# Kernel tuning notes

Measured on AMD Instinct MI355X. Metric: run time of the kernel, lower is better.

Reference implementation:

```python
import jax, jax.numpy as jnp
import numpy as np

IMAGE_H, IMAGE_W = 256, 704
Z, Y, X = 128, 8, 128
BOUNDS = (-50.0, 50.0, -5.0, 5.0, -50.0, 50.0)
CENTROID = (0.0, 1.0, 0.0)
EPS_MEAN = 1e-6
EPS_DEPTH = 1e-4


def _compose_rt(R, t):
    M = jnp.zeros(R.shape[:-2] + (4, 4), R.dtype)
    M = M.at[..., :3, :3].set(R)
    M = M.at[..., :3, 3].set(t)
    M = M.at[..., 3, 3].set(1.0)
    return M


def _safe_inverse(M):
    R = M[..., :3, :3]
    t = M[..., :3, 3]
    Rt = jnp.swapaxes(R, -1, -2)
    return _compose_rt(Rt, -jnp.einsum('...ij,...j->...i', Rt, t))


def _apply_4x4(M, xyz):
    # M: (...,4,4), xyz: (...,N,3) -> (...,N,3)
    return jnp.einsum('...ij,...nj->...ni', M[..., :3, :3], xyz) + M[..., None, :3, 3]


def _xyz_camA():
    # Mem2Ref of gridcloud3d: x_ref = x_mem*vox + MIN + vox/2 (bounds shifted by centroid)
    xmin = BOUNDS[0] + CENTROID[0]; xmax = BOUNDS[1] + CENTROID[0]
    ymin = BOUNDS[2] + CENTROID[1]; ymax = BOUNDS[3] + CENTROID[1]
    zmin = BOUNDS[4] + CENTROID[2]; zmax = BOUNDS[5] + CENTROID[2]
    vx = (xmax - xmin) / X; vy = (ymax - ymin) / Y; vz = (zmax - zmin) / Z
    zz, yy, xx = jnp.meshgrid(jnp.arange(Z, dtype=jnp.float32),
                              jnp.arange(Y, dtype=jnp.float32),
                              jnp.arange(X, dtype=jnp.float32), indexing='ij')
    x = xx * vx + xmin + vx / 2.0
    y = yy * vy + ymin + vy / 2.0
    z = zz * vz + zmin + vz / 2.0
    return jnp.stack([x, y, z], -1).reshape(Z * Y * X, 3)  # mem order (Z,Y,X)


def _bilinear_sample(img, px, py):
    # img: (C,H,W); px,py: (N,) pixel coords; zeros padding (grid_sample align_corners=False)
    C, H, W = img.shape
    x0 = jnp.floor(px); y0 = jnp.floor(py)
    dx = px - x0; dy = py - y0
    x0i = x0.astype(jnp.int32); y0i = y0.astype(jnp.int32)
    flat = img.reshape(C, H * W)

    def gather(yi, xi, w):
        inb = (xi >= 0) & (xi < W) & (yi >= 0) & (yi < H)
        idx = jnp.clip(yi, 0, H - 1) * W + jnp.clip(xi, 0, W - 1)
        return flat[:, idx] * (w * inb.astype(img.dtype))

    return (gather(y0i, x0i, (1 - dx) * (1 - dy))
            + gather(y0i, x0i + 1, dx * (1 - dy))
            + gather(y0i + 1, x0i, (1 - dx) * dy)
            + gather(y0i + 1, x0i + 1, dx * dy))  # (C,N)


def _forward(cam_feat, camera2ego, cam_intrinsic, conv_w):
    B, S, C, Hf, Wf = cam_feat.shape
    # velo_T_cams = merge_rt(camera2ego R, t); cam0_T_camXs = inv(velo_T_cams[:,0]) @ velo_T_cams
    velo_T_cams = _compose_rt(camera2ego[..., :3, :3], camera2ego[..., :3, 3])
    cam0_T_velo = _safe_inverse(velo_T_cams[:, 0])
    cam0_T_camXs = jnp.einsum('bij,bsjk->bsik', cam0_T_velo, velo_T_cams)
    camXs_T_cam0 = _safe_inverse(cam0_T_camXs)
    # scale_intrinsics with sy = Hf/H*0.284, sx = Wf/W*0.44
    sy = Hf / float(IMAGE_H) * 0.284
    sx = Wf / float(IMAGE_W) * 0.44
    fx = cam_intrinsic[..., 0, 0] * sx
    fy = cam_intrinsic[..., 1, 1] * sy
    cx = cam_intrinsic[..., 0, 2] * sx
    cy = cam_intrinsic[..., 1, 2] * sy
    K = jnp.zeros((B, S, 4, 4), cam_feat.dtype)
    K = K.at[..., 0, 0].set(fx).at[..., 1, 1].set(fy)
    K = K.at[..., 0, 2].set(cx).at[..., 1, 2].set(cy)
    K = K.at[..., 2, 2].set(1.0).at[..., 3, 3].set(1.0)
    pixB_T_cam0 = jnp.einsum('bsij,bsjk->bsik', K, camXs_T_cam0)

    xyz = _xyz_camA()  # (N,3), N = Z*Y*X
    xyz_camB = _apply_4x4(camXs_T_cam0, xyz[None, None])  # (B,S,N,3)
    z_cam = xyz_camB[..., 2]
    xyz_pix = _apply_4x4(pixB_T_cam0, xyz[None, None])
    depth = jnp.maximum(xyz_pix[..., 2], EPS_DEPTH)
    x_pix = xyz_pix[..., 0] / depth
    y_pix = xyz_pix[..., 1] / depth
    valid = ((x_pix > -0.5) & (x_pix < Wf - 0.5)
             & (y_pix > -0.5) & (y_pix < Hf - 0.5)
             & (z_cam > 0.0)).astype(cam_feat.dtype)
    # normalize_grid2d (clamp [-2,2]) then grid_sample align_corners=False unnormalize
    gx = jnp.clip(2.0 * x_pix / (Wf - 1) - 1.0, -2.0, 2.0)
    gy = jnp.clip(2.0 * y_pix / (Hf - 1) - 1.0, -2.0, 2.0)
    px = ((gx + 1.0) * Wf - 1.0) / 2.0
    py = ((gy + 1.0) * Hf - 1.0) / 2.0

    feats = cam_feat.reshape(B * S, C, Hf, Wf)
    vals = jax.vmap(_bilinear_sample)(feats, px.reshape(B * S, -1), py.reshape(B * S, -1))
    vals = vals.reshape(B, S, C, -1) * valid[:, :, None, :]  # (B,S,C,N)
    mask = (jnp.abs(vals) > 0).astype(vals.dtype)
    feat_mem = jnp.sum(vals * mask, axis=1) / (EPS_MEAN + jnp.sum(mask, axis=1))  # (B,C,N)
    feat_mem = feat_mem.reshape(B, C, Z, Y, X)

    # BEV compress: permute(0,1,3,2,4) -> (B, C*Y, Z, X), conv3x3 (no bias), InstanceNorm2d, GELU
    feat_bev = jnp.transpose(feat_mem, (0, 1, 3, 2, 4)).reshape(B, C * Y, Z, X)
    out = jax.lax.conv_general_dilated(feat_bev, conv_w, (1, 1), ((1, 1), (1, 1)),
                                       dimension_numbers=('NCHW', 'OIHW', 'NCHW'))
    mu = jnp.mean(out, axis=(2, 3), keepdims=True)
    var = jnp.var(out, axis=(2, 3), keepdims=True)
    out = (out - mu) / jnp.sqrt(var + 1e-5)
    return jax.nn.gelu(out, approximate=False)


def setup_inputs() -> dict:
    key = jax.random.key(0)
    k1, k2, k3 = jax.random.split(key, 3)
    B, S, C, Hf, Wf = 1, 6, 128, 32, 88
    cam_feat = jax.random.normal(k1, (B, S, C, Hf, Wf), jnp.float32)
    # rigid camera2ego: yaw rotations about the y axis + small translations
    yaws = jnp.arange(S, dtype=jnp.float32) * (2.0 * jnp.pi / S)
    c, s = jnp.cos(yaws), jnp.sin(yaws)
    zr, on = jnp.zeros_like(c), jnp.ones_like(c)
    R = jnp.stack([jnp.stack([c, zr, s], -1),
                   jnp.stack([zr, on, zr], -1),
                   jnp.stack([-s, zr, c], -1)], -2)  # (S,3,3)
    t = jax.random.normal(k2, (S, 3), jnp.float32) * 0.5
    cam2ego = jnp.zeros((B, S, 4, 4), jnp.float32)
    cam2ego = cam2ego.at[0, :, :3, :3].set(R).at[0, :, :3, 3].set(t).at[0, :, 3, 3].set(1.0)
    K = jnp.zeros((B, S, 4, 4), jnp.float32)
    K = K.at[..., 0, 0].set(600.0).at[..., 1, 1].set(600.0)
    K = K.at[..., 0, 2].set(352.0).at[..., 1, 2].set(128.0)
    K = K.at[..., 2, 2].set(1.0).at[..., 3, 3].set(1.0)
    conv_w = jax.random.normal(k3, (128, 128 * Y, 3, 3), jnp.float32) / np.sqrt(128 * Y * 9.0).astype(np.float32)
    return {"cam_feat": cam_feat, "camera2ego": cam2ego, "cam_intrinsic": K, "conv_w": conv_w}


def reference(cam_feat, camera2ego, cam_intrinsic, conv_w):
    return _forward(cam_feat, camera2ego, cam_intrinsic, conv_w)
```

## Files before the change

### kernel.cpp

```cpp
#include <hip/hip_runtime.h>
#include <hip/hip_bf16.h>
#include <math.h>

#define HF 32
#define WF 88
#define NCAM 6
#define CC 128
#define ZD 128
#define YD 8
#define XD 128

using f32x4  = __attribute__((ext_vector_type(4))) float;
using bf16x8 = __attribute__((ext_vector_type(8))) short;

#define OFF_P    0ull
#define OFF_W    512ull
#define OFF_CAMT (OFF_W + 2359296ull)
#define OFF_F    (OFF_CAMT + 8650752ull)
#define OFF_CONV (OFF_F + 34611200ull)

__global__ __launch_bounds__(64) void k0_mats(const float* __restrict__ cam2ego,
                                              const float* __restrict__ intr,
                                              float* __restrict__ P) {
  int s = threadIdx.x;
  if (s >= NCAM) return;
  const float* M0 = cam2ego;
  const float* Ms = cam2ego + s * 16;
  float Rb[9], tb[3];
  for (int i = 0; i < 3; i++)
    for (int j = 0; j < 3; j++) {
      float v = 0.f;
      for (int k = 0; k < 3; k++) v += Ms[k * 4 + i] * M0[k * 4 + j];
      Rb[i * 3 + j] = v;
    }
  for (int i = 0; i < 3; i++) {
    float v = 0.f;
    for (int k = 0; k < 3; k++) v += Ms[k * 4 + i] * (M0[k * 4 + 3] - Ms[k * 4 + 3]);
    tb[i] = v;
  }
  const float* Ks = intr + s * 16;
  const float sx = (float)WF / 704.0f * 0.44f;
  const float sy = (float)HF / 256.0f * 0.284f;
  const float fx = Ks[0] * sx, fy = Ks[5] * sy;
  const float cx = Ks[2] * sx, cy = Ks[6] * sy;
  float* p = P + s * 12;
  for (int j = 0; j < 3; j++) p[j]     = fx * Rb[j]     + cx * Rb[6 + j];
  p[3]  = fx * tb[0] + cx * tb[2];
  for (int j = 0; j < 3; j++) p[4 + j] = fy * Rb[3 + j] + cy * Rb[6 + j];
  p[7]  = fy * tb[1] + cy * tb[2];
  for (int j = 0; j < 3; j++) p[8 + j] = Rb[6 + j];
  p[11] = tb[2];
}

__global__ __launch_bounds__(256) void k1_transpose(const float* __restrict__ feat,
                                                    __hip_bfloat16* __restrict__ camT) {
  __shared__ float tile[128 * 89];
  const int b = blockIdx.x;
  const int s = b >> 5;
  const int hrow = b & 31;
  const int t = threadIdx.x;
  for (int idx = t; idx < 128 * 88; idx += 256) {
    const int c = idx / 88;
    const int w = idx - c * 88;
    tile[c * 89 + w] = feat[((size_t)(s * CC + c) * HF + hrow) * WF + w];
  }
  __syncthreads();
  const int c = t & 127;
  const int wh = t >> 7;
  for (int i = 0; i < 44; i++) {
    const int w = i * 2 + wh;
    camT[((size_t)(s * HF + hrow) * WF + w) * CC + c] =
        __float2bfloat16(tile[c * 89 + w]);
  }
}

__global__ __launch_bounds__(256) void k1b_packw(const float* __restrict__ w,
                                                 __hip_bfloat16* __restrict__ wp) {
  const int t = blockIdx.x * 256 + threadIdx.x;
  float v[9];
  #pragma unroll
  for (int d = 0; d < 9; d++) v[d] = w[(size_t)t * 9 + d];
  #pragma unroll
  for (int d = 0; d < 9; d++) wp[(size_t)d * 131072 + t] = __float2bfloat16(v[d]);
}

struct Rec { int off[4]; float w[4]; };

__global__ __launch_bounds__(256) void k2_sample(const __hip_bfloat16* __restrict__ camT,
                                                 const float* __restrict__ P,
                                                 __hip_bfloat16* __restrict__ F) {
  const int bz = blockIdx.x / 65;
  const int bxp = blockIdx.x % 65;
  const int t = threadIdx.x;
  const int sub = t >> 7;
  const int u = t & 127;
  const int bx = bxp * 2 + sub;
  const int zi = bz - 1, xi = bx - 1;
  const int cq = (u & 31) << 2;
  const int yq = u >> 5;
  __hip_bfloat16* Fb = F + ((size_t)bz * 130 + bx) * 1024;
  const bool inplay = !(zi < 0 || zi >= ZD || xi < 0 || xi >= XD);

  __shared__ Rec recs[2][48];
  __shared__ unsigned ymask[2][8];
  const int lane = t & 63;
  const int wv = t >> 6;
  bool vflag = false;
  if ((wv == 0 || wv == 2) && lane < 48 && inplay) {
    const int y = lane / 6, s = lane - y * 6;
    const float* pp = P + s * 12;
    const float vx = 100.0f / 128.0f;
    const float xw = xi * vx - 50.0f + vx * 0.5f;
    const float zw = zi * vx - 50.0f + vx * 0.5f;
    const float yw = y * 1.25f - 4.0f + 0.625f;
    const float zc = pp[8] * xw + pp[9] * yw + pp[10] * zw + pp[11];
    const float xp = pp[0] * xw + pp[1] * yw + pp[2] * zw + pp[3];
    const float yp = pp[4] * xw + pp[5] * yw + pp[6] * zw + pp[7];
    const float dep = fmaxf(zc, 1e-4f);
    const float pxf = xp / dep, pyf = yp / dep;
    const bool valid = (pxf > -0.5f && pxf < (float)WF - 0.5f &&
                        pyf > -0.5f && pyf < (float)HF - 0.5f && zc > 0.0f);
    const float px = pxf * ((float)WF / (float)(WF - 1)) - 0.5f;
    const float py = pyf * ((float)HF / (float)(HF - 1)) - 0.5f;
    const float fx0 = floorf(px), fy0 = floorf(py);
    const float ddx = px - fx0, ddy = py - fy0;
    const int x0i = (int)fx0, y0i = (int)fy0;
    const float vf = valid ? 1.0f : 0.0f;
    float ww[4];
    ww[0] = (1.0f - ddx) * (1.0f - ddy) * vf;
    ww[1] = ddx * (1.0f - ddy) * vf;
    ww[2] = (1.0f - ddx) * ddy * vf;
    ww[3] = ddx * ddy * vf;
    const int cxs[4] = {x0i, x0i + 1, x0i, x0i + 1};
    const int cys[4] = {y0i, y0i, y0i + 1, y0i + 1};
    Rec r;
    float wsum = 0.f;
    #pragma unroll
    for (int k = 0; k < 4; k++) {
      const bool inb = ((unsigned)cxs[k] < WF) && ((unsigned)cys[k] < HF);
      const int xc = min(max(cxs[k], 0), WF - 1);
      const int yc = min(max(cys[k], 0), HF - 1);
      r.w[k] = inb ? ww[k] : 0.0f;
      r.off[k] = (s * (HF * WF) + yc * WF + xc) * CC;
      wsum += r.w[k];
    }
    recs[sub][lane] = r;
    vflag = wsum > 0.0f;
  }
  if (wv == 0 || wv == 2) {
    unsigned long long m = __ballot(vflag);
    if (lane < 8) ymask[wv >> 1][lane] = (unsigned)((m >> (6 * lane)) & 63ull);
  }
  __syncthreads();

  if (!inplay) {
    #pragma unroll
    for (int j = 0; j < 4; j++)
      *reinterpret_cast<unsigned*>(Fb + (cq + j) * 8 + yq * 2) = 0u;
    return;
  }

  float num[2][4] = {{0.f, 0.f, 0.f, 0.f}, {0.f, 0.f, 0.f, 0.f}};
  int cnt[2] = {0, 0};
  #pragma unroll
  for (int yi = 0; yi < 2; yi++) {
    const int y = yq * 2 + yi;
    unsigned ms = ymask[sub][y];
    while (ms) {
      const int s = __builtin_ctz(ms);
      ms &= ms - 1;
      const Rec r = recs[sub][y * 6 + s];
      #pragma unroll
      for (int k = 0; k < 4; k++) {
        const ushort4 uv = *reinterpret_cast<const ushort4*>(&camT[r.off[k] + cq]);
        num[yi][0] += r.w[k] * __bfloat162float(*reinterpret_cast<const __hip_bfloat16*>(&uv.x));
        num[yi][1] += r.w[k] * __bfloat162float(*reinterpret_cast<const __hip_bfloat16*>(&uv.y));
        num[yi][2] += r.w[k] * __bfloat162float(*reinterpret_cast<const __hip_bfloat16*>(&uv.z));
        num[yi][3] += r.w[k] * __bfloat162float(*reinterpret_cast<const __hip_bfloat16*>(&uv.w));
      }
      cnt[yi]++;
    }
  }
  const float inv0 = 1.0f / (1e-6f + (float)cnt[0]);
  const float inv1 = 1.0f / (1e-6f + (float)cnt[1]);
  #pragma unroll
  for (int j = 0; j < 4; j++) {
    __hip_bfloat16 o[2];
    o[0] = __float2bfloat16(num[0][j] * inv0);
    o[1] = __float2bfloat16(num[1][j] * inv1);
    *reinterpret_cast<unsigned*>(Fb + (cq + j) * 8 + yq * 2) =
        *reinterpret_cast<const unsigned*>(o);
  }
}

__device__ __forceinline__ void load_lds16(const void* g, void* l) {
  __builtin_amdgcn_global_load_lds(
      (const __attribute__((address_space(1))) unsigned int*)g,
      (__attribute__((address_space(3))) unsigned int*)l, 16, 0, 0);
}

#define K3_NT 72

__global__ __launch_bounds__(512) void k3_gemm(const __hip_bfloat16* __restrict__ F,
                                               const __hip_bfloat16* __restrict__ Wp,
                                               float* __restrict__ out0,
                                               float* __restrict__ out1) {
  const int orig = (blockIdx.x & 7) * 32 + (blockIdx.x >> 3);
  const int z = orig & 127;
  const int h = orig >> 7;
  const int ciH = h << 9;
  const int tid = threadIdx.x;
  const int w = tid >> 6;
  const int l = tid & 63;
  const int kk = w >> 2;
  const int wq = w & 3;
  const int wm = wq >> 1;
  const int wn = wq & 1;
  __shared__ __hip_bfloat16 lds[4][16384];

  f32x4 acc[4][4];
  #pragma unroll
  for (int m = 0; m < 4; m++)
    #pragma unroll
    for (int n = 0; n < 4; n++)
      acc[m][n] = (f32x4){0.f, 0.f, 0.f, 0.f};

  auto stage = [&](int kt) {
    const int buf = kt & 3;
    const int d = kt >> 3;
    const int dz = d / 3, dx = d - dz * 3;
    const int ci0 = ciH + ((kt & 7) << 6);
    const int zbase = (z + dz) * 130 + dx;
    #pragma unroll
    for (int i = 0; i < 2; i++) {
      const int n = w * 128 + i * 64 + l;
      const int row = n >> 3;
      const int q = (n & 7) ^ (row & 7);
      const __hip_bfloat16* src = F + ((size_t)(zbase + row) << 10) + ci0 + (q << 3);
      load_lds16(src, &lds[buf][(w * 128 + i * 64) * 8]);
    }
    #pragma unroll
    for (int i = 0; i < 2; i++) {
      const int n = w * 128 + i * 64 + l;
      const int co = n >> 3;
      const int q = (n & 7) ^ (co & 7);
      const __hip_bfloat16* src = Wp + ((size_t)d << 17) + ((size_t)co << 10) + ci0 + (q << 3);
      load_lds16(src, &lds[buf][8192 + (w * 128 + i * 64) * 8]);
    }
  };

  auto compute = [&](int kt) {
    const int buf = kt & 3;
    const int r16 = l & 15;
    const int hi = l >> 4;
    const int c = kk * 4 + hi;
    bf16x8 a[4], b[4];
    #pragma unroll
    for (int m = 0; m < 4; m++) {
      const int r = wm * 64 + m * 16 + r16;
      const int slot = c ^ (r & 7);
      a[m] = *reinterpret_cast<const bf16x8*>(&lds[buf][r * 64 + slot * 8]);
    }
    #pragma unroll
    for (int n = 0; n < 4; n++) {
      const int co = wn * 64 + n * 16 + r16;
      const int slot = c ^ (co & 7);
      b[n] = *reinterpret_cast<const bf16x8*>(&lds[buf][8192 + co * 64 + slot * 8]);
    }
    #pragma unroll
    for (int m = 0; m < 4; m++)
      #pragma unroll
      for (int n = 0; n < 4; n++)
        acc[m][n] = __builtin_amdgcn_mfma_f32_16x16x32_bf16(a[m], b[n], acc[m][n], 0, 0, 0);
  };

  stage(0); stage(1); stage(2);

  for (int t = 0; t < K3_NT - 2; ++t) {
    asm volatile("s_waitcnt vmcnt(8)" ::: "memory");
    __builtin_amdgcn_s_barrier();
    if (t + 3 < K3_NT) stage(t + 3);
    compute(t);
  }
  asm volatile("s_waitcnt vmcnt(4)" ::: "memory");
  __builtin_amdgcn_s_barrier();
  compute(K3_NT - 2);
  asm volatile("s_waitcnt vmcnt(0)" ::: "memory");
  __builtin_amdgcn_s_barrier();
  compute(K3_NT - 1);

  float* red = reinterpret_cast<float*>(&lds[0][0]);
  if (kk == 1) {
    float* dst = red + wq * 4096;
    #pragma unroll
    for (int m = 0; m < 4; m++)
      #pragma unroll
      for (int n = 0; n < 4; n++)
        *reinterpret_cast<f32x4*>(&dst[(m * 4 + n) * 256 + l * 4]) = acc[m][n];
  }
  __syncthreads();
  if (kk == 0) {
    const float* srcr = red + wq * 4096;
    float* outP = h ? out1 : out0;
    const int r16 = l & 15;
    const int hi = l >> 4;
    #pragma unroll
    for (int m = 0; m < 4; m++) {
      const int xr = wm * 64 + m * 16 + hi * 4;
      #pragma unroll
      for (int n = 0; n < 4; n++) {
        f32x4 o = *reinterpret_cast<const f32x4*>(&srcr[(m * 4 + n) * 256 + l * 4]);
        f32x4 r = acc[m][n] + o;
        const int co = wn * 64 + n * 16 + r16;
        *reinterpret_cast<f32x4*>(&outP[((size_t)co << 14) + (z << 7) + xr]) = r;
      }
    }
  }
}

__device__ __forceinline__ float gelu_exact(float x) {
  return 0.5f * x * (1.0f + erff(x * 0.70710678118654752440f));
}

__global__ __launch_bounds__(1024) void k4_ln(const float* __restrict__ c0,
                                              const float* __restrict__ c1,
                                              float* __restrict__ outp) {
  const int co = blockIdx.x;
  const int t = threadIdx.x;
  const float4* p0 = reinterpret_cast<const float4*>(c0 + ((size_t)co << 14));
  const float4* p1 = reinterpret_cast<const float4*>(c1 + ((size_t)co << 14));
  float4 v[4];
  float s = 0.f, s2 = 0.f;
  #pragma unroll
  for (int i = 0; i < 4; i++) {
    float4 a = p0[t + (i << 10)];
    float4 b = p1[t + (i << 10)];
    float4 r;
    r.x = a.x + b.x; r.y = a.y + b.y; r.z = a.z + b.z; r.w = a.w + b.w;
    v[i] = r;
    s  += r.x + r.y + r.z + r.w;
    s2 += r.x * r.x + r.y * r.y + r.z * r.z + r.w * r.w;
  }
  #pragma unroll
  for (int off = 32; off > 0; off >>= 1) {
    s  += __shfl_down(s, off);
    s2 += __shfl_down(s2, off);
  }
  __shared__ float red[32];
  __shared__ float mb[2];
  const int wv = t >> 6, ln = t & 63;
  if (ln == 0) { red[wv] = s; red[wv + 16] = s2; }
  __syncthreads();
  if (t == 0) {
    float S = 0.f, S2 = 0.f;
    #pragma unroll
    for (int i = 0; i < 16; i++) { S += red[i]; S2 += red[i + 16]; }
    float mu = S * (1.0f / 16384.0f);
    float var = S2 * (1.0f / 16384.0f) - mu * mu;
    mb[0] = mu;
    mb[1] = 1.0f / sqrtf(var + 1e-5f);
  }
  __syncthreads();
  const float mu = mb[0], inv = mb[1];
  float4* op = reinterpret_cast<float4*>(outp + ((size_t)co << 14));
  #pragma unroll
  for (int i = 0; i < 4; i++) {
    float4 x = v[i];
    float4 r;
    r.x = gelu_exact((x.x - mu) * inv);
    r.y = gelu_exact((x.y - mu) * inv);
    r.z = gelu_exact((x.z - mu) * inv);
    r.w = gelu_exact((x.w - mu) * inv);
    op[t + (i << 10)] = r;
  }
}

extern "C" void kernel_launch(void* const* d_in, const int* in_sizes, int n_in,
                              void* d_out, int out_size, void* d_ws, size_t ws_size,
                              hipStream_t stream) {
  const float* cam_feat = (const float*)d_in[0];
  const float* cam2ego  = (const float*)d_in[1];
  const float* intr     = (const float*)d_in[2];
  const float* conv_w   = (const float*)d_in[3];
  float* out = (float*)d_out;
  char* ws = (char*)d_ws;

  float*          P     = (float*)(ws + OFF_P);
  __hip_bfloat16* Wp    = (__hip_bfloat16*)(ws + OFF_W);
  __hip_bfloat16* camT  = (__hip_bfloat16*)(ws + OFF_CAMT);
  __hip_bfloat16* F     = (__hip_bfloat16*)(ws + OFF_F);
  float*          conv0 = (float*)(ws + OFF_CONV);
  float*          conv1 = (float*)(ws + OFF_CAMT);

  hipLaunchKernelGGL(k0_mats, dim3(1), dim3(64), 0, stream, cam2ego, intr, P);
  hipLaunchKernelGGL(k1_transpose, dim3(NCAM * HF), dim3(256), 0, stream, cam_feat, camT);
  hipLaunchKernelGGL(k1b_packw, dim3(512), dim3(256), 0, stream, conv_w, Wp);
  hipLaunchKernelGGL(k2_sample, dim3(130 * 65), dim3(256), 0, stream, camT, P, F);
  hipLaunchKernelGGL(k3_gemm, dim3(256), dim3(512), 0, stream, F, Wp, conv0, conv1);
  hipLaunchKernelGGL(k4_ln, dim3(128), dim3(1024), 0, stream, conv0, conv1, out);
}
```

Baseline: 111.1 us.

## Merge preprocessing kernels and interleave GEMM staging with split MFMA phases

```diff
diff --git a/kernel.cpp b/kernel.cpp
--- a/kernel.cpp
+++ b/kernel.cpp
@@ -19,69 +19,69 @@
 #define OFF_F    (OFF_CAMT + 8650752ull)
 #define OFF_CONV (OFF_F + 34611200ull)
 
-__global__ __launch_bounds__(64) void k0_mats(const float* __restrict__ cam2ego,
-                                              const float* __restrict__ intr,
-                                              float* __restrict__ P) {
-  int s = threadIdx.x;
-  if (s >= NCAM) return;
-  const float* M0 = cam2ego;
-  const float* Ms = cam2ego + s * 16;
-  float Rb[9], tb[3];
-  for (int i = 0; i < 3; i++)
-    for (int j = 0; j < 3; j++) {
-      float v = 0.f;
-      for (int k = 0; k < 3; k++) v += Ms[k * 4 + i] * M0[k * 4 + j];
-      Rb[i * 3 + j] = v;
-    }
-  for (int i = 0; i < 3; i++) {
-    float v = 0.f;
-    for (int k = 0; k < 3; k++) v += Ms[k * 4 + i] * (M0[k * 4 + 3] - Ms[k * 4 + 3]);
-    tb[i] = v;
-  }
-  const float* Ks = intr + s * 16;
-  const float sx = (float)WF / 704.0f * 0.44f;
-  const float sy = (float)HF / 256.0f * 0.284f;
-  const float fx = Ks[0] * sx, fy = Ks[5] * sy;
-  const float cx = Ks[2] * sx, cy = Ks[6] * sy;
-  float* p = P + s * 12;
-  for (int j = 0; j < 3; j++) p[j]     = fx * Rb[j]     + cx * Rb[6 + j];
-  p[3]  = fx * tb[0] + cx * tb[2];
-  for (int j = 0; j < 3; j++) p[4 + j] = fy * Rb[3 + j] + cy * Rb[6 + j];
-  p[7]  = fy * tb[1] + cy * tb[2];
-  for (int j = 0; j < 3; j++) p[8 + j] = Rb[6 + j];
-  p[11] = tb[2];
-}
-
-__global__ __launch_bounds__(256) void k1_transpose(const float* __restrict__ feat,
-                                                    __hip_bfloat16* __restrict__ camT) {
+__global__ __launch_bounds__(256) void k_pre(const float* __restrict__ feat,
+                                             const float* __restrict__ conv_w,
+                                             const float* __restrict__ cam2ego,
+                                             const float* __restrict__ intr,
+                                             __hip_bfloat16* __restrict__ camT,
+                                             __hip_bfloat16* __restrict__ wp,
+                                             float* __restrict__ P) {
   __shared__ float tile[128 * 89];
   const int b = blockIdx.x;
-  const int s = b >> 5;
-  const int hrow = b & 31;
   const int t = threadIdx.x;
-  for (int idx = t; idx < 128 * 88; idx += 256) {
-    const int c = idx / 88;
-    const int w = idx - c * 88;
-    tile[c * 89 + w] = feat[((size_t)(s * CC + c) * HF + hrow) * WF + w];
-  }
-  __syncthreads();
-  const int c = t & 127;
-  const int wh = t >> 7;
-  for (int i = 0; i < 44; i++) {
-    const int w = i * 2 + wh;
-    camT[((size_t)(s * HF + hrow) * WF + w) * CC + c] =
-        __float2bfloat16(tile[c * 89 + w]);
-  }
-}
-
-__global__ __launch_bounds__(256) void k1b_packw(const float* __restrict__ w,
-                                                 __hip_bfloat16* __restrict__ wp) {
-  const int t = blockIdx.x * 256 + threadIdx.x;
-  float v[9];
-  #pragma unroll
-  for (int d = 0; d < 9; d++) v[d] = w[(size_t)t * 9 + d];
-  #pragma unroll
-  for (int d = 0; d < 9; d++) wp[(size_t)d * 131072 + t] = __float2bfloat16(v[d]);
+  if (b < 192) {
+    const int s = b >> 5;
+    const int hrow = b & 31;
+    for (int idx = t; idx < 128 * 88; idx += 256) {
+      const int c = idx / 88;
+      const int w = idx - c * 88;
+      tile[c * 89 + w] = feat[((size_t)(s * CC + c) * HF + hrow) * WF + w];
+    }
+    __syncthreads();
+    const int c = t & 127;
+    const int wh = t >> 7;
+    for (int i = 0; i < 44; i++) {
+      const int w = i * 2 + wh;
+      camT[((size_t)(s * HF + hrow) * WF + w) * CC + c] =
+          __float2bfloat16(tile[c * 89 + w]);
+    }
+  } else if (b < 704) {
+    const int tt = (b - 192) * 256 + t;
+    float v[9];
+    #pragma unroll
+    for (int d = 0; d < 9; d++) v[d] = conv_w[(size_t)tt * 9 + d];
+    #pragma unroll
+    for (int d = 0; d < 9; d++) wp[(size_t)d * 131072 + tt] = __float2bfloat16(v[d]);
+  } else {
+    const int s = t;
+    if (s >= NCAM) return;
+    const float* M0 = cam2ego;
+    const float* Ms = cam2ego + s * 16;
+    float Rb[9], tb[3];
+    for (int i = 0; i < 3; i++)
+      for (int j = 0; j < 3; j++) {
+        float v = 0.f;
+        for (int k = 0; k < 3; k++) v += Ms[k * 4 + i] * M0[k * 4 + j];
+        Rb[i * 3 + j] = v;
+      }
+    for (int i = 0; i < 3; i++) {
+      float v = 0.f;
+      for (int k = 0; k < 3; k++) v += Ms[k * 4 + i] * (M0[k * 4 + 3] - Ms[k * 4 + 3]);
+      tb[i] = v;
+    }
+    const float* Ks = intr + s * 16;
+    const float sx = (float)WF / 704.0f * 0.44f;
+    const float sy = (float)HF / 256.0f * 0.284f;
+    const float fx = Ks[0] * sx, fy = Ks[5] * sy;
+    const float cx = Ks[2] * sx, cy = Ks[6] * sy;
+    float* p = P + s * 12;
+    for (int j = 0; j < 3; j++) p[j]     = fx * Rb[j]     + cx * Rb[6 + j];
+    p[3]  = fx * tb[0] + cx * tb[2];
+    for (int j = 0; j < 3; j++) p[4 + j] = fy * Rb[3 + j] + cy * Rb[6 + j];
+    p[7]  = fy * tb[1] + cy * tb[2];
+    for (int j = 0; j < 3; j++) p[8 + j] = Rb[6 + j];
+    p[11] = tb[2];
+  }
 }
 
 struct Rec { int off[4]; float w[4]; };
@@ -225,7 +225,7 @@
     for (int n = 0; n < 4; n++)
       acc[m][n] = (f32x4){0.f, 0.f, 0.f, 0.f};
 
-  auto stage = [&](int kt) {
+  auto stage_A = [&](int kt) {
     const int buf = kt & 3;
     const int d = kt >> 3;
     const int dz = d / 3, dx = d - dz * 3;
@@ -239,6 +239,11 @@
       const __hip_bfloat16* src = F + ((size_t)(zbase + row) << 10) + ci0 + (q << 3);
       load_lds16(src, &lds[buf][(w * 128 + i * 64) * 8]);
     }
+  };
+  auto stage_B = [&](int kt) {
+    const int buf = kt & 3;
+    const int d = kt >> 3;
+    const int ci0 = ciH + ((kt & 7) << 6);
     #pragma unroll
     for (int i = 0; i < 2; i++) {
       const int n = w * 128 + i * 64 + l;
@@ -249,45 +254,64 @@
     }
   };
 
-  auto compute = [&](int kt) {
-    const int buf = kt & 3;
-    const int r16 = l & 15;
-    const int hi = l >> 4;
-    const int c = kk * 4 + hi;
+  const int r16 = l & 15;
+  const int hi = l >> 4;
+  const int cslot = kk * 4 + hi;
+
+  auto step = [&](int t, bool doStage, int wcode) {
+    const int buf = t & 3;
     bf16x8 a[4], b[4];
     #pragma unroll
     for (int m = 0; m < 4; m++) {
       const int r = wm * 64 + m * 16 + r16;
-      const int slot = c ^ (r & 7);
+      const int slot = cslot ^ (r & 7);
       a[m] = *reinterpret_cast<const bf16x8*>(&lds[buf][r * 64 + slot * 8]);
     }
     #pragma unroll
-    for (int n = 0; n < 4; n++) {
+    for (int n = 0; n < 2; n++) {
       const int co = wn * 64 + n * 16 + r16;
-      const int slot = c ^ (co & 7);
+      const int slot = cslot ^ (co & 7);
       b[n] = *reinterpret_cast<const bf16x8*>(&lds[buf][8192 + co * 64 + slot * 8]);
     }
-    #pragma unroll
-    for (int m = 0; m < 4; m++)
-      #pragma unroll
-      for (int n = 0; n < 4; n++)
-        acc[m][n] = __builtin_amdgcn_mfma_f32_16x16x32_bf16(a[m], b[n], acc[m][n], 0, 0, 0);
+    if (doStage) stage_A(t + 3);
+    __builtin_amdgcn_s_barrier();
+    __builtin_amdgcn_s_setprio(1);
+    #pragma unroll
+    for (int m = 0; m < 4; m++) {
+      acc[m][0] = __builtin_amdgcn_mfma_f32_16x16x32_bf16(a[m], b[0], acc[m][0], 0, 0, 0);
+      acc[m][1] = __builtin_amdgcn_mfma_f32_16x16x32_bf16(a[m], b[1], acc[m][1], 0, 0, 0);
+    }
+    __builtin_amdgcn_s_setprio(0);
+    __builtin_amdgcn_s_barrier();
+    #pragma unroll
+    for (int n = 2; n < 4; n++) {
+      const int co = wn * 64 + n * 16 + r16;
+      const int slot = cslot ^ (co & 7);
+      b[n] = *reinterpret_cast<const bf16x8*>(&lds[buf][8192 + co * 64 + slot * 8]);
+    }
+    if (doStage) stage_B(t + 3);
+    __builtin_amdgcn_s_barrier();
+    __builtin_amdgcn_s_setprio(1);
+    #pragma unroll
+    for (int m = 0; m < 4; m++) {
+      acc[m][2] = __builtin_amdgcn_mfma_f32_16x16x32_bf16(a[m], b[2], acc[m][2], 0, 0, 0);
+      acc[m][3] = __builtin_amdgcn_mfma_f32_16x16x32_bf16(a[m], b[3], acc[m][3], 0, 0, 0);
+    }
+    __builtin_amdgcn_s_setprio(0);
+    if (wcode == 8)      asm volatile("s_waitcnt vmcnt(8)" ::: "memory");
+    else if (wcode == 4) asm volatile("s_waitcnt vmcnt(4)" ::: "memory");
+    else if (wcode == 0) asm volatile("s_waitcnt vmcnt(0)" ::: "memory");
+    __builtin_amdgcn_s_barrier();
   };
 
-  stage(0); stage(1); stage(2);
-
-  for (int t = 0; t < K3_NT - 2; ++t) {
-    asm volatile("s_waitcnt vmcnt(8)" ::: "memory");
-    __builtin_amdgcn_s_barrier();
-    if (t + 3 < K3_NT) stage(t + 3);
-    compute(t);
-  }
-  asm volatile("s_waitcnt vmcnt(4)" ::: "memory");
+  stage_A(0); stage_B(0); stage_A(1); stage_B(1); stage_A(2); stage_B(2);
+  asm volatile("s_waitcnt vmcnt(8)" ::: "memory");
   __builtin_amdgcn_s_barrier();
-  compute(K3_NT - 2);
-  asm volatile("s_waitcnt vmcnt(0)" ::: "memory");
-  __builtin_amdgcn_s_barrier();
-  compute(K3_NT - 1);
+
+  for (int t = 0; t < K3_NT - 3; ++t) step(t, true, 8);
+  step(K3_NT - 3, false, 4);
+  step(K3_NT - 2, false, 0);
+  step(K3_NT - 1, false, -1);
 
   float* red = reinterpret_cast<float*>(&lds[0][0]);
   if (kk == 1) {
@@ -302,8 +326,6 @@
   if (kk == 0) {
     const float* srcr = red + wq * 4096;
     float* outP = h ? out1 : out0;
-    const int r16 = l & 15;
-    const int hi = l >> 4;
     #pragma unroll
     for (int m = 0; m < 4; m++) {
       const int xr = wm * 64 + m * 16 + hi * 4;
@@ -392,9 +414,8 @@
   float*          conv0 = (float*)(ws + OFF_CONV);
   float*          conv1 = (float*)(ws + OFF_CAMT);
 
-  hipLaunchKernelGGL(k0_mats, dim3(1), dim3(64), 0, stream, cam2ego, intr, P);
-  hipLaunchKernelGGL(k1_transpose, dim3(NCAM * HF), dim3(256), 0, stream, cam_feat, camT);
-  hipLaunchKernelGGL(k1b_packw, dim3(512), dim3(256), 0, stream, conv_w, Wp);
+  hipLaunchKernelGGL(k_pre, dim3(705), dim3(256), 0, stream,
+                     cam_feat, conv_w, cam2ego, intr, camT, Wp, P);
   hipLaunchKernelGGL(k2_sample, dim3(130 * 65), dim3(256), 0, stream, camT, P, F);
   hipLaunchKernelGGL(k3_gemm, dim3(256), dim3(512), 0, stream, F, Wp, conv0, conv1);
   hipLaunchKernelGGL(k4_ln, dim3(128), dim3(1024), 0, stream, conv0, conv1, out);
```

Result: faster. 104.0 us (-6.4%).
